# Optimization experiments

Hardware: AMD Instinct MI355X
Metric: run time of the kernel (lower is better)

## Reference

```python
import math
import jax, jax.numpy as jnp
from jax import lax
import numpy as np

C, H, W, N, K = 256, 64, 64, 16, 7

def setup_inputs() -> dict:
    key = jax.random.key(0)
    k0, k1, k2, k3, k4 = jax.random.split(key, 5)
    x = jax.random.normal(k0, (N, C, H, W), dtype=jnp.float32)
    p_2_w = 0.02 * jax.random.normal(k1, (1, C, H, 1), dtype=jnp.float32)
    # nn.Conv2d(c, c, (1,5), groups=1, bias=False) -> weight [c, c, 1, 5]
    fan_in = C * 1 * 5
    bound = 1.0 / math.sqrt(fan_in)
    p_3_w = jax.random.uniform(k2, (C, C, 1, 5), dtype=jnp.float32, minval=-bound, maxval=bound)
    p_4_w = 0.02 * jax.random.normal(k3, (1, C, K, 1, 1), dtype=jnp.float32)
    p_6_w = jax.random.uniform(k4, (K, 1), dtype=jnp.float32, minval=-7.0, maxval=7.0)
    return {"x": x, "p_2_w": p_2_w, "p_3_w": p_3_w, "p_4_w": p_4_w, "p_6_w": p_6_w}

def reference(x, p_2_w, p_3_w, p_4_w, p_6_w):
    n, c, h, w = x.shape
    k = p_4_w.shape[2]  # 7 taps
    pad = (k - 1) // 2
    # F.unfold with kernel (1,7), pad (0,3): stack 7 width-shifted copies -> [n,c,7,h,w]
    xp = jnp.pad(x, ((0, 0), (0, 0), (0, 0), (pad, pad)))
    t_1 = jnp.stack([xp[..., i:i + w] for i in range(k)], axis=2)
    # per-(channel,row) scaling then dense 1x5 conv
    t_2 = p_2_w * x
    t_3 = lax.conv_general_dilated(
        t_2, p_3_w, window_strides=(1, 1), padding=[(0, 0), (2, 2)],
        dimension_numbers=("NCHW", "OIHW", "NCHW"))
    # weighted tap-sum: (p_4_w * t_1) contracted over taps with p_6_w[:,0]
    t_4 = p_4_w * t_1
    t_6 = jnp.einsum("nckhw,kf->ncfhw", t_4, p_6_w)[:, :, 0]  # [n,c,h,w]
    t_5 = jax.nn.relu(x)
    s = h * w
    # channel-attention matrix [n,c,c]
    t_7 = jnp.einsum("ncs,nds->ncd", t_3.reshape(n, c, s), t_6.reshape(n, c, s))
    t_7 = t_7 * (1.0 / math.sqrt(s))
    # bmm(t_5^T, t_7) -> [n,s,d]; permuting to [n,d,h,w] == einsum 'ncs,ncd->nds'
    out = jnp.einsum("ncs,ncd->nds", t_5.reshape(n, c, s), t_7)
    out = out * (1.0 / math.sqrt(c))
    return out.reshape(n, c, h, w)
```

## Files before the change

### kernel.cpp

```cpp
#include <hip/hip_runtime.h>
#include <hip/hip_bf16.h>

typedef __attribute__((ext_vector_type(8))) short bf16x8;
typedef __attribute__((ext_vector_type(4))) float f32x4;

#define NB 16
#define CD 256
#define HD 64
#define WD 64
#define WP 68
#define SD 4096
#define KU 1280

__device__ __forceinline__ void gload16(const void* g, void* lds) {
  __builtin_amdgcn_global_load_lds(
      (const __attribute__((address_space(1))) unsigned int*)g,
      (__attribute__((address_space(3))) unsigned int*)lds, 16, 0, 0);
}

__global__ __launch_bounds__(256) void prep_w3(const float* __restrict__ p3,
                                               __hip_bfloat16* __restrict__ A) {
  int id = blockIdx.x * 256 + threadIdx.x;
  if (id >= CD * KU) return;
  int o = id / KU;
  int r = id - o * KU;
  int j = r >> 8;
  int c = r & 255;
  A[id] = __float2bfloat16(p3[(o * CD + c) * 5 + j]);
}

__global__ __launch_bounds__(256) void prep_x(const float* __restrict__ x,
                                              const float* __restrict__ p2,
                                              const float* __restrict__ p4,
                                              const float* __restrict__ p6,
                                              __hip_bfloat16* __restrict__ t2p,
                                              __hip_bfloat16* __restrict__ t5T,
                                              __hip_bfloat16* __restrict__ t6) {
  int h = blockIdx.x;
  int c0 = blockIdx.y * 64;
  int n = blockIdx.z;
  __shared__ float xl[64][67];
  __shared__ float p2l[64];
  __shared__ float wtl[64][8];
  int t = threadIdx.x;

  if (t < 64) p2l[t] = p2[(c0 + t) * HD + h];
  for (int idx = t; idx < 448; idx += 256) {
    int c = idx / 7, k = idx - c * 7;
    wtl[c][k] = p4[(c0 + c) * 7 + k] * p6[k];
  }

  {
    int cq = t >> 4;
    int w4 = (t & 15) * 4;
#pragma unroll
    for (int cc = 0; cc < 4; ++cc) {
      int cl = cc * 16 + cq;
      const float4 xv = *reinterpret_cast<const float4*>(
          &x[(((size_t)n * CD + c0 + cl) * HD + h) * WD + w4]);
      xl[cl][w4 + 0] = xv.x;
      xl[cl][w4 + 1] = xv.y;
      xl[cl][w4 + 2] = xv.z;
      xl[cl][w4 + 3] = xv.w;
    }
  }
  __syncthreads();

  __hip_bfloat16* t2pn = t2p + (size_t)n * HD * WP * CD;
#pragma unroll
  for (int ii = 0; ii < 2; ++ii) {
    int w = (t >> 3) + ii * 32;
    int cb = (t & 7) * 8;
    __hip_bfloat16 o2[8], o5[8];
#pragma unroll
    for (int j = 0; j < 8; ++j) {
      float xv = xl[cb + j][w];
      o5[j] = __float2bfloat16(fmaxf(xv, 0.f));
      o2[j] = __float2bfloat16(p2l[cb + j] * xv);
    }
    size_t s = (size_t)h * 64 + w;
    *reinterpret_cast<bf16x8*>(&t5T[((size_t)n * SD + s) * CD + c0 + cb]) =
        *reinterpret_cast<const bf16x8*>(o5);
    *reinterpret_cast<bf16x8*>(&t2pn[((size_t)h * WP + w + 2) * CD + c0 + cb]) =
        *reinterpret_cast<const bf16x8*>(o2);
  }
  if (t < 32) {
    int pi = t >> 3;
    int wp = (pi < 2) ? pi : pi + 64;
    int cb = (t & 7) * 8;
    bf16x8 z = (bf16x8){0, 0, 0, 0, 0, 0, 0, 0};
    *reinterpret_cast<bf16x8*>(&t2pn[((size_t)h * WP + wp) * CD + c0 + cb]) = z;
  }

#pragma unroll
  for (int ii = 0; ii < 2; ++ii) {
    int cl = (t >> 3) + ii * 32;
    int w8 = (t & 7) * 8;
    float hx[14];
#pragma unroll
    for (int m = 0; m < 14; ++m) {
      int wi = w8 - 3 + m;
      hx[m] = (wi >= 0 && wi < 64) ? xl[cl][wi] : 0.f;
    }
    float wt[7];
#pragma unroll
    for (int k = 0; k < 7; ++k) wt[k] = wtl[cl][k];
    __hip_bfloat16 o6[8];
#pragma unroll
    for (int u = 0; u < 8; ++u) {
      float acc = 0.f;
#pragma unroll
      for (int k = 0; k < 7; ++k) acc += wt[k] * hx[u + k];
      o6[u] = __float2bfloat16(acc);
    }
    *reinterpret_cast<bf16x8*>(&t6[((size_t)n * CD + c0 + cl) * SD + h * 64 + w8]) =
        *reinterpret_cast<const bf16x8*>(o6);
  }
}

#define STAGE_A(c, kt, d)                                                              \
  gload16(Ab + (size_t)((c) * 64 + wv * 8 + (lane >> 3)) * 2560 + (kt) * 128 + cbsrc,  \
          (char*)lds + (d) * 65536 + (c) * 8192 + wv * 1024)
#define STAGE_B(j, kt, d)                                                              \
  gload16(t2pb + (size_t)(s0 + (j) * 64 + wv * 8 + (lane >> 3) + 4 * (sb * 4 + (j))) * 512 + \
                     (kt) * 128 + cbsrc,                                               \
          (char*)lds + (d) * 65536 + 32768 + (j) * 8192 + wv * 1024)

#define LOAD_AV(d, MH)                                                                 \
  do {                                                                                 \
    const __hip_bfloat16* pA =                                                         \
        lds + (d) * 32768 + (wm * 128 + (MH) * 64 + l16) * 64;                         \
    _Pragma("unroll") for (int ks = 0; ks < 2; ++ks) {                                 \
      int cb = (ks * 32 + lg * 8) ^ lxor;                                              \
      _Pragma("unroll") for (int mf = 0; mf < 4; ++mf)                                 \
          av[ks * 4 + mf] = *reinterpret_cast<const bf16x8*>(pA + mf * 1024 + cb);     \
    }                                                                                  \
  } while (0)

#define QUADR(d, MH, NH)                                                               \
  do {                                                                                 \
    const __hip_bfloat16* pB =                                                         \
        lds + (d) * 32768 + 16384 + (wn * 64 + (NH) * 32 + l16) * 64;                  \
    bf16x8 bv[4];                                                                      \
    _Pragma("unroll") for (int ks = 0; ks < 2; ++ks) {                                 \
      int cb = (ks * 32 + lg * 8) ^ lxor;                                              \
      _Pragma("unroll") for (int nf = 0; nf < 2; ++nf)                                 \
          bv[ks * 2 + nf] = *reinterpret_cast<const bf16x8*>(pB + nf * 1024 + cb);     \
    }                                                                                  \
    __builtin_amdgcn_s_setprio(1);                                                     \
    _Pragma("unroll") for (int ks = 0; ks < 2; ++ks)                                   \
        _Pragma("unroll") for (int mf = 0; mf < 4; ++mf)                               \
            _Pragma("unroll") for (int nf = 0; nf < 2; ++nf)                           \
                acc[(MH) * 4 + mf][(NH) * 2 + nf] = __builtin_amdgcn_mfma_f32_16x16x32_bf16( \
                    av[ks * 4 + mf], bv[ks * 2 + nf], acc[(MH) * 4 + mf][(NH) * 2 + nf], \
                    0, 0, 0);                                                          \
    __builtin_amdgcn_s_setprio(0);                                                     \
  } while (0)

#define VMWAIT(N) asm volatile("s_waitcnt vmcnt(" #N ")" ::: "memory")
#define BARRIER() __builtin_amdgcn_s_barrier()

__global__ __launch_bounds__(512, 2) void gemm_b8(const __hip_bfloat16* __restrict__ A,
                                                  const __hip_bfloat16* __restrict__ t2p,
                                                  __hip_bfloat16* __restrict__ t3) {
  __shared__ __align__(16) __hip_bfloat16 lds[65536];
  const int n = blockIdx.z;
  const int sb = blockIdx.x;
  const int t = threadIdx.x;
  const int wv = t >> 6, lane = t & 63;
  const int wm = wv >> 2, wn = wv & 3;
  const int l16 = lane & 15, lg = lane >> 4;
  const int s0 = sb * 256;
  const char* Ab = (const char*)A;
  const char* t2pb = (const char*)(t2p + (size_t)n * HD * WP * CD);
  const int cbsrc = ((lane & 7) ^ (lane >> 3)) * 16;
  const int lxor = (l16 & 7) * 8;

  f32x4 acc[8][4];
#pragma unroll
  for (int i = 0; i < 8; ++i)
#pragma unroll
    for (int j = 0; j < 4; ++j) acc[i][j] = (f32x4){0.f, 0.f, 0.f, 0.f};

  bf16x8 av[8];

  STAGE_B(0, 0, 0); STAGE_B(1, 0, 0); STAGE_B(2, 0, 0); STAGE_B(3, 0, 0);
  STAGE_A(0, 0, 0); STAGE_A(2, 0, 0); STAGE_A(1, 0, 0); STAGE_A(3, 0, 0);

  for (int kt = 0; kt < 19; ++kt) {
    const int cur = kt & 1, nxt = cur ^ 1, kn = kt + 1;
    STAGE_B(0, kn, nxt); STAGE_B(1, kn, nxt);
    VMWAIT(4);
    BARRIER();
    LOAD_AV(cur, 0);
    QUADR(cur, 0, 0);
    BARRIER();
    STAGE_B(2, kn, nxt); STAGE_B(3, kn, nxt);
    BARRIER();
    QUADR(cur, 0, 1);
    BARRIER();
    STAGE_A(0, kn, nxt); STAGE_A(2, kn, nxt);
    VMWAIT(6);
    BARRIER();
    LOAD_AV(cur, 1);
    QUADR(cur, 1, 0);
    BARRIER();
    STAGE_A(1, kn, nxt); STAGE_A(3, kn, nxt);
    BARRIER();
    QUADR(cur, 1, 1);
    BARRIER();
  }
  VMWAIT(2);
  BARRIER();
  LOAD_AV(1, 0);
  QUADR(1, 0, 0);
  BARRIER();
  BARRIER();
  QUADR(1, 0, 1);
  BARRIER();
  VMWAIT(0);
  BARRIER();
  LOAD_AV(1, 1);
  QUADR(1, 1, 0);
  BARRIER();
  BARRIER();
  QUADR(1, 1, 1);
  BARRIER();

  __hip_bfloat16* t3n = t3 + (size_t)n * CD * SD;
#pragma unroll
  for (int im = 0; im < 8; ++im)
#pragma unroll
    for (int in = 0; in < 4; ++in) {
      int row0 = wm * 128 + im * 16 + lg * 4;
      int col = s0 + wn * 64 + in * 16 + l16;
#pragma unroll
      for (int r = 0; r < 4; ++r)
        t3n[(size_t)(row0 + r) * SD + col] = __float2bfloat16(acc[im][in][r]);
    }
}

__global__ __launch_bounds__(256) void gemm_c_part(const __hip_bfloat16* __restrict__ t6,
                                                   const __hip_bfloat16* __restrict__ t3,
                                                   float* __restrict__ P4) {
  __shared__ __align__(16) __hip_bfloat16 lA[64 * 64];
  __shared__ __align__(16) __hip_bfloat16 lB[64 * 64];
  int bx = blockIdx.x;
  int cbk = bx & 3, kc = bx >> 2;
  int db = blockIdx.y;
  int n = blockIdx.z;
  int t = threadIdx.x;
  int wave = t >> 6, lane = t & 63;
  int wm = wave >> 1, wn = wave & 1;
  int l16 = lane & 15, lg = lane >> 4;
  int d0 = db * 64;
  int c0 = cbk * 64;
  int kbase = kc * 1024;
  const __hip_bfloat16* An = t6 + (size_t)n * CD * SD + kbase;
  const __hip_bfloat16* Bn = t3 + (size_t)n * CD * SD + kbase;

  int srow = t >> 3;
  int scol = (t & 7) * 8;
  const __hip_bfloat16* gA0 = An + (size_t)(d0 + srow) * SD + scol;
  const __hip_bfloat16* gA1 = An + (size_t)(d0 + srow + 32) * SD + scol;
  const __hip_bfloat16* gB0 = Bn + (size_t)(c0 + srow) * SD + scol;
  const __hip_bfloat16* gB1 = Bn + (size_t)(c0 + srow + 32) * SD + scol;
  __hip_bfloat16* lAd0 = &lA[t * 8];
  __hip_bfloat16* lAd1 = &lA[t * 8 + 32 * 64];
  __hip_bfloat16* lBd0 = &lB[t * 8];
  __hip_bfloat16* lBd1 = &lB[t * 8 + 32 * 64];

  f32x4 acc[2][2];
#pragma unroll
  for (int mi = 0; mi < 2; ++mi)
#pragma unroll
    for (int ni = 0; ni < 2; ++ni) acc[mi][ni] = (f32x4){0.f, 0.f, 0.f, 0.f};

  gload16(gA0, lAd0);
  gload16(gA1, lAd1);
  gload16(gB0, lBd0);
  gload16(gB1, lBd1);

  for (int k = 0; k < 16; ++k) {
    __syncthreads();
#pragma unroll
    for (int ks = 0; ks < 2; ++ks) {
      bf16x8 a[2], b[2];
#pragma unroll
      for (int mi = 0; mi < 2; ++mi)
        a[mi] = *reinterpret_cast<const bf16x8*>(&lA[(wm * 32 + mi * 16 + l16) * 64 + ks * 32 + lg * 8]);
#pragma unroll
      for (int ni = 0; ni < 2; ++ni)
        b[ni] = *reinterpret_cast<const bf16x8*>(&lB[(wn * 32 + ni * 16 + l16) * 64 + ks * 32 + lg * 8]);
#pragma unroll
      for (int mi = 0; mi < 2; ++mi)
#pragma unroll
        for (int ni = 0; ni < 2; ++ni)
          acc[mi][ni] = __builtin_amdgcn_mfma_f32_16x16x32_bf16(a[mi], b[ni], acc[mi][ni], 0, 0, 0);
    }
    __syncthreads();
    if (k < 15) {
      int kk = (k + 1) * 64;
      gload16(gA0 + kk, lAd0);
      gload16(gA1 + kk, lAd1);
      gload16(gB0 + kk, lBd0);
      gload16(gB1 + kk, lBd1);
    }
  }

  float* Pn = P4 + ((size_t)kc * NB + n) * CD * CD;
#pragma unroll
  for (int mi = 0; mi < 2; ++mi)
#pragma unroll
    for (int ni = 0; ni < 2; ++ni) {
      int col = c0 + wn * 32 + ni * 16 + l16;
      int row0 = d0 + wm * 32 + mi * 16 + lg * 4;
#pragma unroll
      for (int r = 0; r < 4; ++r)
        Pn[(size_t)(row0 + r) * CD + col] = acc[mi][ni][r];
    }
}

__global__ __launch_bounds__(256) void reduce_P(const float* __restrict__ P4,
                                                __hip_bfloat16* __restrict__ P) {
  size_t i = ((size_t)blockIdx.x * 256 + threadIdx.x) * 4;
  const size_t stride = (size_t)NB * CD * CD;
  float4 a = *reinterpret_cast<const float4*>(P4 + i);
  float4 b = *reinterpret_cast<const float4*>(P4 + stride + i);
  float4 c = *reinterpret_cast<const float4*>(P4 + 2 * stride + i);
  float4 d = *reinterpret_cast<const float4*>(P4 + 3 * stride + i);
  __hip_bfloat16 o[4];
  o[0] = __float2bfloat16((a.x + b.x + c.x + d.x) * 0.015625f);
  o[1] = __float2bfloat16((a.y + b.y + c.y + d.y) * 0.015625f);
  o[2] = __float2bfloat16((a.z + b.z + c.z + d.z) * 0.015625f);
  o[3] = __float2bfloat16((a.w + b.w + c.w + d.w) * 0.015625f);
  *reinterpret_cast<short4*>(&P[i]) = *reinterpret_cast<const short4*>(o);
}

#define DSTAGE_A(i, kk)                                                                \
  gload16(Pb + (size_t)((i) * 32 + wv4 * 8 + (lane >> 3)) * 512 + (kk) * 128 + cbsrc,  \
          (char*)lA + (i) * 4096 + wv4 * 1024)
#define DSTAGE_B(i, kk)                                                                \
  gload16(Tb + (size_t)(s0 + (i) * 32 + wv4 * 8 + (lane >> 3)) * 512 + (kk) * 128 + cbsrc, \
          (char*)lB + (i) * 4096 + wv4 * 1024)

__global__ __launch_bounds__(256, 2) void gemm_d(const __hip_bfloat16* __restrict__ P,
                                                 const __hip_bfloat16* __restrict__ t5T,
                                                 float* __restrict__ out) {
  __shared__ __align__(16) __hip_bfloat16 lA[256 * 64];
  __shared__ __align__(16) __hip_bfloat16 lB[128 * 64];
  const int n = blockIdx.z;
  const int sb = blockIdx.x;
  const int t = threadIdx.x;
  const int wv4 = t >> 6, lane = t & 63;
  const int wm = wv4 >> 1, wn = wv4 & 1;
  const int l16 = lane & 15, lg = lane >> 4;
  const int s0 = sb * 128;
  const char* Pb = (const char*)(P + (size_t)n * CD * CD);
  const char* Tb = (const char*)(t5T + (size_t)n * SD * CD);
  const int cbsrc = ((lane & 7) ^ (lane >> 3)) * 16;
  const int lxor = (l16 & 7) * 8;

  f32x4 acc[8][4];
#pragma unroll
  for (int i = 0; i < 8; ++i)
#pragma unroll
    for (int j = 0; j < 4; ++j) acc[i][j] = (f32x4){0.f, 0.f, 0.f, 0.f};

#pragma unroll
  for (int i = 0; i < 8; ++i) DSTAGE_A(i, 0);
#pragma unroll
  for (int i = 0; i < 4; ++i) DSTAGE_B(i, 0);

  for (int k = 0; k < 4; ++k) {
    __syncthreads();
#pragma unroll
    for (int ks = 0; ks < 2; ++ks) {
      int cb = (ks * 32 + lg * 8) ^ lxor;
      bf16x8 a[8], b[4];
#pragma unroll
      for (int mf = 0; mf < 8; ++mf)
        a[mf] = *reinterpret_cast<const bf16x8*>(&lA[(wm * 128 + mf * 16 + l16) * 64 + cb]);
#pragma unroll
      for (int nf = 0; nf < 4; ++nf)
        b[nf] = *reinterpret_cast<const bf16x8*>(&lB[(wn * 64 + nf * 16 + l16) * 64 + cb]);
#pragma unroll
      for (int mf = 0; mf < 8; ++mf)
#pragma unroll
        for (int nf = 0; nf < 4; ++nf)
          acc[mf][nf] = __builtin_amdgcn_mfma_f32_16x16x32_bf16(a[mf], b[nf], acc[mf][nf], 0, 0, 0);
    }
    __syncthreads();
    if (k < 3) {
      int kk = k + 1;
#pragma unroll
      for (int i = 0; i < 8; ++i) DSTAGE_A(i, kk);
#pragma unroll
      for (int i = 0; i < 4; ++i) DSTAGE_B(i, kk);
    }
  }

  float* outn = out + (size_t)n * CD * SD;
#pragma unroll
  for (int mf = 0; mf < 8; ++mf)
#pragma unroll
    for (int nf = 0; nf < 4; ++nf) {
      int col = s0 + wn * 64 + nf * 16 + l16;
      int row0 = wm * 128 + mf * 16 + lg * 4;
#pragma unroll
      for (int r = 0; r < 4; ++r)
        outn[(size_t)(row0 + r) * SD + col] = acc[mf][nf][r] * 0.0625f;
    }
}

extern "C" void kernel_launch(void* const* d_in, const int* in_sizes, int n_in,
                              void* d_out, int out_size, void* d_ws, size_t ws_size,
                              hipStream_t stream) {
  const float* x = (const float*)d_in[0];
  const float* p2 = (const float*)d_in[1];
  const float* p3 = (const float*)d_in[2];
  const float* p4 = (const float*)d_in[3];
  const float* p6 = (const float*)d_in[4];

  char* ws = (char*)d_ws;
  size_t off = 0;
  __hip_bfloat16* A = (__hip_bfloat16*)(ws + off);
  off += (size_t)CD * KU * 2;
  size_t t2p_off = off;
  __hip_bfloat16* t2p = (__hip_bfloat16*)(ws + off);
  off += (size_t)NB * HD * WP * CD * 2;
  __hip_bfloat16* t5T = (__hip_bfloat16*)(ws + off);
  off += (size_t)NB * SD * CD * 2;
  __hip_bfloat16* t6 = (__hip_bfloat16*)(ws + off);
  off += (size_t)NB * CD * SD * 2;
  __hip_bfloat16* t3 = (__hip_bfloat16*)(ws + off);
  off += (size_t)NB * CD * SD * 2;
  float* P4 = (float*)(ws + t2p_off);
  __hip_bfloat16* P = (__hip_bfloat16*)(ws + t2p_off + (size_t)4 * NB * CD * CD * 4);

  float* out = (float*)d_out;

  prep_w3<<<dim3((CD * KU + 255) / 256), 256, 0, stream>>>(p3, A);
  prep_x<<<dim3(HD, 4, NB), 256, 0, stream>>>(x, p2, p4, p6, t2p, t5T, t6);
  gemm_b8<<<dim3(16, 1, NB), 512, 0, stream>>>(A, t2p, t3);
  gemm_c_part<<<dim3(16, 4, NB), 256, 0, stream>>>(t6, t3, P4);
  reduce_P<<<dim3((NB * CD * CD / 4) / 256), 256, 0, stream>>>(P4, P);
  gemm_d<<<dim3(32, 1, NB), 256, 0, stream>>>(P, t5T, out);
}
```

Measured before the change: 133.3 us.

## Double-buffer LDS fragments in registers and cut barriers in bf16 GEMM loop

Restructures the main GEMM K-loop so the A/B fragments for the next quadrant and the next K tile are read from LDS into separate register sets (av0/av1, bvA/bvB) ahead of the MFMAs that use them. All B and all A global-to-LDS stages for the next tile are issued in two batches, with a single full vmcnt wait per iteration instead of the earlier partial waits. This should overlap LDS reads with MFMA work and lower the barrier count per iteration. In exchange it holds many more live fragment registers, which risks spills or lower occupancy under the (512,2) launch bound, and the full wait at the end of each iteration may expose global-load latency.

```diff
diff --git a/kernel.cpp b/kernel.cpp
--- a/kernel.cpp
+++ b/kernel.cpp
@@ -126,33 +126,36 @@
                      (kt) * 128 + cbsrc,                                               \
           (char*)lds + (d) * 65536 + 32768 + (j) * 8192 + wv * 1024)
 
-#define LOAD_AV(d, MH)                                                                 \
+#define LDAV(d, MH, AV)                                                                \
   do {                                                                                 \
     const __hip_bfloat16* pA =                                                         \
         lds + (d) * 32768 + (wm * 128 + (MH) * 64 + l16) * 64;                         \
     _Pragma("unroll") for (int ks = 0; ks < 2; ++ks) {                                 \
       int cb = (ks * 32 + lg * 8) ^ lxor;                                              \
       _Pragma("unroll") for (int mf = 0; mf < 4; ++mf)                                 \
-          av[ks * 4 + mf] = *reinterpret_cast<const bf16x8*>(pA + mf * 1024 + cb);     \
+          AV[ks * 4 + mf] = *reinterpret_cast<const bf16x8*>(pA + mf * 1024 + cb);     \
     }                                                                                  \
   } while (0)
 
-#define QUADR(d, MH, NH)                                                               \
+#define LDBV(d, NH, BV)                                                                \
   do {                                                                                 \
     const __hip_bfloat16* pB =                                                         \
         lds + (d) * 32768 + 16384 + (wn * 64 + (NH) * 32 + l16) * 64;                  \
-    bf16x8 bv[4];                                                                      \
     _Pragma("unroll") for (int ks = 0; ks < 2; ++ks) {                                 \
       int cb = (ks * 32 + lg * 8) ^ lxor;                                              \
       _Pragma("unroll") for (int nf = 0; nf < 2; ++nf)                                 \
-          bv[ks * 2 + nf] = *reinterpret_cast<const bf16x8*>(pB + nf * 1024 + cb);     \
+          BV[ks * 2 + nf] = *reinterpret_cast<const bf16x8*>(pB + nf * 1024 + cb);     \
     }                                                                                  \
+  } while (0)
+
+#define MFMAQ(MH, NH, AV, BV)                                                          \
+  do {                                                                                 \
     __builtin_amdgcn_s_setprio(1);                                                     \
     _Pragma("unroll") for (int ks = 0; ks < 2; ++ks)                                   \
         _Pragma("unroll") for (int mf = 0; mf < 4; ++mf)                               \
             _Pragma("unroll") for (int nf = 0; nf < 2; ++nf)                           \
                 acc[(MH) * 4 + mf][(NH) * 2 + nf] = __builtin_amdgcn_mfma_f32_16x16x32_bf16( \
-                    av[ks * 4 + mf], bv[ks * 2 + nf], acc[(MH) * 4 + mf][(NH) * 2 + nf], \
+                    AV[ks * 4 + mf], BV[ks * 2 + nf], acc[(MH) * 4 + mf][(NH) * 2 + nf], \
                     0, 0, 0);                                                          \
     __builtin_amdgcn_s_setprio(0);                                                     \
   } while (0)
@@ -182,50 +185,39 @@
 #pragma unroll
     for (int j = 0; j < 4; ++j) acc[i][j] = (f32x4){0.f, 0.f, 0.f, 0.f};
 
-  bf16x8 av[8];
+  bf16x8 av0[8], av1[8], bvA[4], bvB[4];
 
   STAGE_B(0, 0, 0); STAGE_B(1, 0, 0); STAGE_B(2, 0, 0); STAGE_B(3, 0, 0);
-  STAGE_A(0, 0, 0); STAGE_A(2, 0, 0); STAGE_A(1, 0, 0); STAGE_A(3, 0, 0);
+  STAGE_A(0, 0, 0); STAGE_A(1, 0, 0); STAGE_A(2, 0, 0); STAGE_A(3, 0, 0);
+  VMWAIT(0);
+  BARRIER();
+  LDAV(0, 0, av0);
+  LDBV(0, 0, bvA);
 
   for (int kt = 0; kt < 19; ++kt) {
     const int cur = kt & 1, nxt = cur ^ 1, kn = kt + 1;
-    STAGE_B(0, kn, nxt); STAGE_B(1, kn, nxt);
-    VMWAIT(4);
+    LDAV(cur, 1, av1);
+    LDBV(cur, 1, bvB);
+    MFMAQ(0, 0, av0, bvA);
+    STAGE_B(0, kn, nxt); STAGE_B(1, kn, nxt); STAGE_B(2, kn, nxt); STAGE_B(3, kn, nxt);
     BARRIER();
-    LOAD_AV(cur, 0);
-    QUADR(cur, 0, 0);
+    MFMAQ(0, 1, av0, bvB);
+    STAGE_A(0, kn, nxt); STAGE_A(1, kn, nxt); STAGE_A(2, kn, nxt); STAGE_A(3, kn, nxt);
     BARRIER();
-    STAGE_B(2, kn, nxt); STAGE_B(3, kn, nxt);
+    MFMAQ(1, 0, av1, bvA);
     BARRIER();
-    QUADR(cur, 0, 1);
+    MFMAQ(1, 1, av1, bvB);
+    VMWAIT(0);
     BARRIER();
-    STAGE_A(0, kn, nxt); STAGE_A(2, kn, nxt);
-    VMWAIT(6);
-    BARRIER();
-    LOAD_AV(cur, 1);
-    QUADR(cur, 1, 0);
-    BARRIER();
-    STAGE_A(1, kn, nxt); STAGE_A(3, kn, nxt);
-    BARRIER();
-    QUADR(cur, 1, 1);
-    BARRIER();
-  }
-  VMWAIT(2);
-  BARRIER();
-  LOAD_AV(1, 0);
-  QUADR(1, 0, 0);
-  BARRIER();
-  BARRIER();
-  QUADR(1, 0, 1);
-  BARRIER();
-  VMWAIT(0);
-  BARRIER();
-  LOAD_AV(1, 1);
-  QUADR(1, 1, 0);
-  BARRIER();
-  BARRIER();
-  QUADR(1, 1, 1);
-  BARRIER();
+    LDAV(nxt, 0, av0);
+    LDBV(nxt, 0, bvA);
+  }
+  LDAV(1, 1, av1);
+  LDBV(1, 1, bvB);
+  MFMAQ(0, 0, av0, bvA);
+  MFMAQ(0, 1, av0, bvB);
+  MFMAQ(1, 0, av1, bvA);
+  MFMAQ(1, 1, av1, bvB);
 
   __hip_bfloat16* t3n = t3 + (size_t)n * CD * SD;
 #pragma unroll
```

New measurement: 133.3 us. Within noise of the previous version (+0.0%).
